# Performance work log

Hardware: AMD Instinct MI355X
Metric: run time of the kernel (lower is better)

The kernel has to match this reference:

```python
import jax, jax.numpy as jnp
import numpy as np
from jax import lax

D_MODEL = 512; D_FF = 2048
D_STATE = 16; D_CONV = 4; EXPAND = 2          # mamba_ssm defaults
D_INNER = EXPAND * D_MODEL                    # 1024
DT_RANK = (D_MODEL + 15) // 16                # 32
B, W, C, D = 2, 1024, 64, 8                   # C*D == D_MODEL


def setup_inputs():
    key = jax.random.key(0)
    ks = jax.random.split(key, 24)
    def p(k, shape, s=0.02):
        return jax.random.normal(k, shape, jnp.float32) * s
    inp = {"x": jax.random.normal(ks[0], (B, W, C, D), jnp.float32)}
    for i, pref in enumerate(["fm", "bm"]):
        o = 1 + i * 7
        inp[pref + "_in_W"] = p(ks[o], (2 * D_INNER, D_MODEL))
        inp[pref + "_conv_W"] = p(ks[o + 1], (D_INNER, D_CONV))
        inp[pref + "_conv_b"] = jnp.zeros((D_INNER,), jnp.float32)
        inp[pref + "_xproj_W"] = p(ks[o + 2], (DT_RANK + 2 * D_STATE, D_INNER))
        inp[pref + "_dt_W"] = p(ks[o + 3], (D_INNER, DT_RANK))
        inp[pref + "_dt_b"] = p(ks[o + 4], (D_INNER,), 0.1)
        inp[pref + "_A_log"] = jnp.log(jnp.broadcast_to(
            jnp.arange(1, D_STATE + 1, dtype=jnp.float32), (D_INNER, D_STATE)))
        inp[pref + "_D"] = jnp.ones((D_INNER,), jnp.float32)
        inp[pref + "_out_W"] = p(ks[o + 5], (D_MODEL, D_INNER))
    inp["ln1_g"] = jnp.ones((D_MODEL,), jnp.float32); inp["ln1_b"] = jnp.zeros((D_MODEL,), jnp.float32)
    inp["ln2_g"] = jnp.ones((D_MODEL,), jnp.float32); inp["ln2_b"] = jnp.zeros((D_MODEL,), jnp.float32)
    inp["ln3_g"] = jnp.ones((D_MODEL,), jnp.float32); inp["ln3_b"] = jnp.zeros((D_MODEL,), jnp.float32)
    inp["ff_W1"] = p(ks[15], (D_FF, D_MODEL)); inp["ff_b1"] = jnp.zeros((D_FF,), jnp.float32)
    inp["ff_W2"] = p(ks[16], (D_MODEL, D_FF)); inp["ff_b2"] = jnp.zeros((D_MODEL,), jnp.float32)
    return inp


def _silu(x):
    return x * jax.nn.sigmoid(x)


def _layernorm(x, g, b, eps=1e-5):
    mu = jnp.mean(x, -1, keepdims=True)
    var = jnp.var(x, -1, keepdims=True)
    return (x - mu) * lax.rsqrt(var + eps) * g + b


def _mamba(u, in_W, conv_W, conv_b, xproj_W, dt_W, dt_b, A_log, Dp, out_W):
    # u: (B, L, d_model). Standard Mamba block (mamba_ssm reference math).
    xz = jnp.einsum('bld,ed->ble', u, in_W)            # (B, L, 2*d_inner)
    xm, z = jnp.split(xz, 2, axis=-1)
    # causal depthwise conv along L
    xc = lax.conv_general_dilated(
        xm.transpose(0, 2, 1), conv_W[:, None, :], (1,),
        [(D_CONV - 1, 0)], feature_group_count=D_INNER)
    xm = _silu((xc + conv_b[None, :, None]).transpose(0, 2, 1))  # (B, L, d_inner)
    dbc = jnp.einsum('bld,ed->ble', xm, xproj_W)       # (B, L, dt_rank + 2*d_state)
    dt = dbc[..., :DT_RANK]
    Bm = dbc[..., DT_RANK:DT_RANK + D_STATE]           # (B, L, d_state)
    Cm = dbc[..., DT_RANK + D_STATE:]                  # (B, L, d_state)
    delta = jax.nn.softplus(jnp.einsum('blr,dr->bld', dt, dt_W) + dt_b)  # (B, L, d_inner)
    A = -jnp.exp(A_log)                                # (d_inner, d_state)
    dA = jnp.exp(delta[..., None] * A)                 # (B, L, d_inner, d_state)
    dBu = delta[..., None] * Bm[:, :, None, :] * xm[..., None]

    def step(h, inputs):
        dA_t, dBu_t = inputs
        h = dA_t * h + dBu_t
        return h, h

    h0 = jnp.zeros((u.shape[0], D_INNER, D_STATE), u.dtype)
    _, hs = lax.scan(step, h0, (dA.transpose(1, 0, 2, 3), dBu.transpose(1, 0, 2, 3)))
    y = jnp.einsum('lbds,lbs->bld', hs, Cm.transpose(1, 0, 2))
    y = y + xm * Dp
    y = y * _silu(z)
    return jnp.einsum('ble,de->bld', y, out_W)         # (B, L, d_model)


def reference(x,
              fm_in_W, fm_conv_W, fm_conv_b, fm_xproj_W, fm_dt_W, fm_dt_b, fm_A_log, fm_D, fm_out_W,
              bm_in_W, bm_conv_W, bm_conv_b, bm_xproj_W, bm_dt_W, bm_dt_b, bm_A_log, bm_D, bm_out_W,
              ln1_g, ln1_b, ln2_g, ln2_b, ln3_g, ln3_b,
              ff_W1, ff_b1, ff_W2, ff_b2):
    b, w, c, d = x.shape
    xf = x.reshape(b, w, c * d)
    fwd = _mamba(xf, fm_in_W, fm_conv_W, fm_conv_b, fm_xproj_W, fm_dt_W, fm_dt_b, fm_A_log, fm_D, fm_out_W)
    bwd = jnp.flip(_mamba(jnp.flip(xf, 1), bm_in_W, bm_conv_W, bm_conv_b, bm_xproj_W,
                          bm_dt_W, bm_dt_b, bm_A_log, bm_D, bm_out_W), 1)
    an1 = _layernorm(xf + fwd, ln1_g, ln1_b)   # AddNorm: LN(x + dropout(y)); dropout off at eval
    an2 = _layernorm(xf + bwd, ln2_g, ln2_b)
    out = an1 + an2
    h = jnp.maximum(jnp.einsum('bld,fd->blf', out, ff_W1) + ff_b1, 0)
    ff = jnp.einsum('blf,df->bld', h, ff_W2) + ff_b2
    out = _layernorm(ff + ff, ln3_g, ln3_b)    # an3(out, out) == LN(out + out)
    return out.reshape(b, w, c, d)
```

## Files before the change

### kernel.cpp

```cpp
#include <hip/hip_runtime.h>
#include <hip/hip_bf16.h>
#include <math.h>

#define MM 2048
#define BATCH 2
#define SEQ 1024
#define DMODEL 512
#define DINNER 1024
#define DSTATE 16
#define DTRANK 32
#define DFF 2048

#define NCHUNK 16
#define CHUNK 64
#define GTOT 65536

typedef short bf16x8 __attribute__((ext_vector_type(8)));
typedef float floatx4 __attribute__((ext_vector_type(4)));
typedef unsigned short ushort8v __attribute__((ext_vector_type(8)));
typedef unsigned short ushort4v __attribute__((ext_vector_type(4)));

__device__ __forceinline__ unsigned short f2bf(float f) {
    union { float f; unsigned u; } v; v.f = f;
    unsigned r = v.u + 0x7FFF + ((v.u >> 16) & 1);
    return (unsigned short)(r >> 16);
}
__device__ __forceinline__ float bf2f(unsigned short u) {
    union { unsigned u; float f; } v; v.u = ((unsigned)u) << 16; return v.f;
}

__device__ __forceinline__ float quadsum4(float x) {
    union { float f; int i; } a, b;
    a.f = x;
    b.i = __builtin_amdgcn_update_dpp(0, a.i, 0xB1, 0xF, 0xF, false); a.f += b.f;
    b.i = __builtin_amdgcn_update_dpp(0, a.i, 0x4E, 0xF, 0xF, false); a.f += b.f;
    return a.f;
}

#define GLOAD_LDS16(gp, lp) __builtin_amdgcn_global_load_lds( \
    (const __attribute__((address_space(1))) unsigned int*)(gp), \
    (__attribute__((address_space(3))) unsigned int*)(lp), 16, 0, 0)


template<int EPI, int OUTBF16>
__global__ __launch_bounds__(256) void gemm_mfma_batch(
    int M, int N, int K,
    const unsigned short* __restrict__ A0, const unsigned short* __restrict__ A1, int lda,
    const unsigned short* __restrict__ B0, const unsigned short* __restrict__ B1, int ldb,
    const float* __restrict__ bias,
    void* __restrict__ C0, void* __restrict__ C1, int ldc)
{
    __shared__ unsigned short As[2][128 * 32];
    __shared__ unsigned short Bs[2][128 * 32];
    const int z = blockIdx.z;
    const unsigned short* A = z ? A1 : A0;
    const unsigned short* B = z ? B1 : B0;
    void* Cout = z ? C1 : C0;
    const int tid  = threadIdx.x;
    const int wave = tid >> 6;
    const int lane = tid & 63;
    const int bm = blockIdx.y * 128;
    const int bn = blockIdx.x * 128;

    const int strow = lane & 15;
    const int stkc  = lane >> 4;
    const int wr = wave >> 1, wc = wave & 1;
    const int frow = lane & 15;
    const int fkc  = lane >> 4;

    floatx4 acc[4][4];
    #pragma unroll
    for (int i = 0; i < 4; ++i)
        #pragma unroll
        for (int j = 0; j < 4; ++j)
            acc[i][j] = (floatx4){0.f, 0.f, 0.f, 0.f};

    for (int k0 = 0; k0 < K; k0 += 64) {
        __syncthreads();
        #pragma unroll
        for (int hh = 0; hh < 2; ++hh) {
            #pragma unroll
            for (int q = 0; q < 2; ++q) {
                int g = wave * 2 + q;
                GLOAD_LDS16(A + (size_t)(bm + g * 16 + strow) * lda + k0 + hh * 32 + stkc * 8,
                            As[hh] + g * 512);
            }
            #pragma unroll
            for (int q = 0; q < 2; ++q) {
                int g = wave * 2 + q;
                GLOAD_LDS16(B + (size_t)(bn + g * 16 + strow) * ldb + k0 + hh * 32 + stkc * 8,
                            Bs[hh] + g * 512);
            }
        }
        __syncthreads();

        #pragma unroll
        for (int hh = 0; hh < 2; ++hh) {
            bf16x8 af[4], bfr[4];
            #pragma unroll
            for (int i = 0; i < 4; ++i)
                af[i] = *(const bf16x8*)(As[hh] + (wr * 4 + i) * 512 + fkc * 128 + frow * 8);
            #pragma unroll
            for (int j = 0; j < 4; ++j)
                bfr[j] = *(const bf16x8*)(Bs[hh] + (wc * 4 + j) * 512 + fkc * 128 + frow * 8);
            #pragma unroll
            for (int i = 0; i < 4; ++i)
                #pragma unroll
                for (int j = 0; j < 4; ++j)
                    acc[i][j] = __builtin_amdgcn_mfma_f32_16x16x32_bf16(
                        af[i], bfr[j], acc[i][j], 0, 0, 0);
        }
    }

    const int orow0 = bm + wr * 64 + (lane >> 4) * 4;
    const int ocol0 = bn + wc * 64 + (lane & 15);
    #pragma unroll
    for (int j = 0; j < 4; ++j) {
        const int col = ocol0 + j * 16;
        const float bv = bias ? bias[col] : 0.f;
        #pragma unroll
        for (int i = 0; i < 4; ++i) {
            #pragma unroll
            for (int r = 0; r < 4; ++r) {
                int row = orow0 + i * 16 + r;
                float t = acc[i][j][r] + bv;
                if (EPI == 1) t = fmaxf(t, 0.f);
                if (OUTBF16)
                    ((unsigned short*)Cout)[(size_t)row * ldc + col] = f2bf(t);
                else
                    ((float*)Cout)[(size_t)row * ldc + col] = t;
            }
        }
    }
}

__global__ __launch_bounds__(256) void gemm_inproj_kernel(
    const unsigned short* __restrict__ A,
    const unsigned short* __restrict__ B0, const unsigned short* __restrict__ B1,
    float* __restrict__ Cx0, float* __restrict__ Cz0,
    float* __restrict__ Cx1, float* __restrict__ Cz1)
{
    __shared__ unsigned short As[2][128 * 32];
    __shared__ unsigned short Bs[2][128 * 32];
    const int z = blockIdx.z;
    const unsigned short* B = z ? B1 : B0;
    const int tid  = threadIdx.x;
    const int wave = tid >> 6;
    const int lane = tid & 63;
    const int bm = blockIdx.y * 128;
    const int bn = blockIdx.x * 128;

    const int strow = lane & 15;
    const int stkc  = lane >> 4;
    const int wr = wave >> 1, wc = wave & 1;
    const int frow = lane & 15;
    const int fkc  = lane >> 4;

    floatx4 acc[4][4];
    #pragma unroll
    for (int i = 0; i < 4; ++i)
        #pragma unroll
        for (int j = 0; j < 4; ++j)
            acc[i][j] = (floatx4){0.f, 0.f, 0.f, 0.f};

    for (int k0 = 0; k0 < DMODEL; k0 += 64) {
        __syncthreads();
        #pragma unroll
        for (int hh = 0; hh < 2; ++hh) {
            #pragma unroll
            for (int q = 0; q < 2; ++q) {
                int g = wave * 2 + q;
                GLOAD_LDS16(A + (size_t)(bm + g * 16 + strow) * DMODEL + k0 + hh * 32 + stkc * 8,
                            As[hh] + g * 512);
            }
            #pragma unroll
            for (int q = 0; q < 2; ++q) {
                int g = wave * 2 + q;
                GLOAD_LDS16(B + (size_t)(bn + g * 16 + strow) * DMODEL + k0 + hh * 32 + stkc * 8,
                            Bs[hh] + g * 512);
            }
        }
        __syncthreads();

        #pragma unroll
        for (int hh = 0; hh < 2; ++hh) {
            bf16x8 af[4], bfr[4];
            #pragma unroll
            for (int i = 0; i < 4; ++i)
                af[i] = *(const bf16x8*)(As[hh] + (wr * 4 + i) * 512 + fkc * 128 + frow * 8);
            #pragma unroll
            for (int j = 0; j < 4; ++j)
                bfr[j] = *(const bf16x8*)(Bs[hh] + (wc * 4 + j) * 512 + fkc * 128 + frow * 8);
            #pragma unroll
            for (int i = 0; i < 4; ++i)
                #pragma unroll
                for (int j = 0; j < 4; ++j)
                    acc[i][j] = __builtin_amdgcn_mfma_f32_16x16x32_bf16(
                        af[i], bfr[j], acc[i][j], 0, 0, 0);
        }
    }

    const int zh = bn >= DINNER;
    float* C = z ? (zh ? Cz1 : Cx1) : (zh ? Cz0 : Cx0);
    const int cb = zh ? DINNER : 0;
    const int orow0 = bm + wr * 64 + (lane >> 4) * 4;
    const int ocol0 = bn + wc * 64 + (lane & 15) - cb;
    #pragma unroll
    for (int j = 0; j < 4; ++j) {
        const int col = ocol0 + j * 16;
        #pragma unroll
        for (int i = 0; i < 4; ++i)
            #pragma unroll
            for (int r = 0; r < 4; ++r)
                C[(size_t)(orow0 + i * 16 + r) * DINNER + col] = acc[i][j][r];
    }
}

template<int NSPLIT>
__global__ __launch_bounds__(256) void gemm_mfma_splitk(
    int M, int N, int K,
    const unsigned short* __restrict__ A0, const unsigned short* __restrict__ A1, int lda,
    const unsigned short* __restrict__ B0, const unsigned short* __restrict__ B1, int ldb,
    float* __restrict__ part, int ldc)
{
    __shared__ unsigned short As[2][128 * 32];
    __shared__ unsigned short Bs[2][128 * 32];
    const int z = blockIdx.z;
    const int dir = z / NSPLIT, sp = z % NSPLIT;
    const unsigned short* A = dir ? A1 : A0;
    const unsigned short* B = dir ? B1 : B0;
    float* Cp = part + (size_t)z * M * ldc;
    const int kbeg = sp * (K / NSPLIT);
    const int kend = kbeg + (K / NSPLIT);
    const int tid  = threadIdx.x;
    const int wave = tid >> 6;
    const int lane = tid & 63;
    const int bm = blockIdx.y * 128;
    const int bn = blockIdx.x * 128;

    const int strow = lane & 15;
    const int stkc  = lane >> 4;
    const int wr = wave >> 1, wc = wave & 1;
    const int frow = lane & 15;
    const int fkc  = lane >> 4;

    floatx4 acc[4][4];
    #pragma unroll
    for (int i = 0; i < 4; ++i)
        #pragma unroll
        for (int j = 0; j < 4; ++j)
            acc[i][j] = (floatx4){0.f, 0.f, 0.f, 0.f};

    for (int k0 = kbeg; k0 < kend; k0 += 64) {
        __syncthreads();
        #pragma unroll
        for (int hh = 0; hh < 2; ++hh) {
            #pragma unroll
            for (int q = 0; q < 2; ++q) {
                int g = wave * 2 + q;
                GLOAD_LDS16(A + (size_t)(bm + g * 16 + strow) * lda + k0 + hh * 32 + stkc * 8,
                            As[hh] + g * 512);
            }
            #pragma unroll
            for (int q = 0; q < 2; ++q) {
                int g = wave * 2 + q;
                GLOAD_LDS16(B + (size_t)(bn + g * 16 + strow) * ldb + k0 + hh * 32 + stkc * 8,
                            Bs[hh] + g * 512);
            }
        }
        __syncthreads();

        #pragma unroll
        for (int hh = 0; hh < 2; ++hh) {
            bf16x8 af[4], bfr[4];
            #pragma unroll
            for (int i = 0; i < 4; ++i)
                af[i] = *(const bf16x8*)(As[hh] + (wr * 4 + i) * 512 + fkc * 128 + frow * 8);
            #pragma unroll
            for (int j = 0; j < 4; ++j)
                bfr[j] = *(const bf16x8*)(Bs[hh] + (wc * 4 + j) * 512 + fkc * 128 + frow * 8);
            #pragma unroll
            for (int i = 0; i < 4; ++i)
                #pragma unroll
                for (int j = 0; j < 4; ++j)
                    acc[i][j] = __builtin_amdgcn_mfma_f32_16x16x32_bf16(
                        af[i], bfr[j], acc[i][j], 0, 0, 0);
        }
    }

    const int orow0 = bm + wr * 64 + (lane >> 4) * 4;
    const int ocol0 = bn + wc * 64 + (lane & 15);
    #pragma unroll
    for (int j = 0; j < 4; ++j) {
        const int col = ocol0 + j * 16;
        #pragma unroll
        for (int i = 0; i < 4; ++i)
            #pragma unroll
            for (int r = 0; r < 4; ++r)
                Cp[(size_t)(orow0 + i * 16 + r) * ldc + col] = acc[i][j][r];
    }
}

__global__ __launch_bounds__(256) void xproj_splitk_kernel(
    const unsigned short* __restrict__ A_f, const unsigned short* __restrict__ A_b,
    const unsigned short* __restrict__ Wf,  const unsigned short* __restrict__ Wb,
    float* __restrict__ part)
{
    __shared__ unsigned short As[2][128 * 32];
    __shared__ unsigned short Bs[2][64 * 32];
    const int tid = threadIdx.x, wave = tid >> 6, lane = tid & 63;
    const int bm = blockIdx.x * 128;
    const int dir = blockIdx.y >> 2, sp = blockIdx.y & 3;
    const unsigned short* A = dir ? A_b : A_f;
    const unsigned short* W = dir ? Wb  : Wf;
    float* Cp = part + (size_t)blockIdx.y * MM * 64;
    const int kbeg = sp * 256, kend = kbeg + 256;

    const int strow = lane & 15;
    const int stkc  = lane >> 4;
    const int frow = lane & 15;
    const int fkc  = lane >> 4;

    floatx4 acc[2][4];
    #pragma unroll
    for (int i = 0; i < 2; ++i)
        #pragma unroll
        for (int j = 0; j < 4; ++j)
            acc[i][j] = (floatx4){0.f, 0.f, 0.f, 0.f};

    for (int k0 = kbeg; k0 < kend; k0 += 64) {
        __syncthreads();
        #pragma unroll
        for (int hh = 0; hh < 2; ++hh) {
            #pragma unroll
            for (int q = 0; q < 2; ++q) {
                int g = wave * 2 + q;
                GLOAD_LDS16(A + (size_t)(bm + g * 16 + strow) * DINNER + k0 + hh * 32 + stkc * 8,
                            As[hh] + g * 512);
            }
            GLOAD_LDS16(W + (size_t)(wave * 16 + strow) * DINNER + k0 + hh * 32 + stkc * 8,
                        Bs[hh] + wave * 512);
        }
        __syncthreads();

        #pragma unroll
        for (int hh = 0; hh < 2; ++hh) {
            bf16x8 af[2], bfr[4];
            #pragma unroll
            for (int i = 0; i < 2; ++i)
                af[i] = *(const bf16x8*)(As[hh] + (wave * 2 + i) * 512 + fkc * 128 + frow * 8);
            #pragma unroll
            for (int j = 0; j < 4; ++j)
                bfr[j] = *(const bf16x8*)(Bs[hh] + j * 512 + fkc * 128 + frow * 8);
            #pragma unroll
            for (int i = 0; i < 2; ++i)
                #pragma unroll
                for (int j = 0; j < 4; ++j)
                    acc[i][j] = __builtin_amdgcn_mfma_f32_16x16x32_bf16(
                        af[i], bfr[j], acc[i][j], 0, 0, 0);
        }
    }

    const int orow0 = bm + wave * 32 + (lane >> 4) * 4;
    #pragma unroll
    for (int j = 0; j < 4; ++j) {
        const int col = (lane & 15) + j * 16;
        #pragma unroll
        for (int i = 0; i < 2; ++i)
            #pragma unroll
            for (int r = 0; r < 4; ++r)
                Cp[(size_t)(orow0 + i * 16 + r) * 64 + col] = acc[i][j][r];
    }
}

__global__ __launch_bounds__(256) void xproj_reduce_kernel(
    const float* __restrict__ part,
    float* __restrict__ dbc_f, float* __restrict__ dbc_b,
    float* __restrict__ bct_f, float* __restrict__ bct_b)
{
    const int dir = blockIdx.y;
    const int i = (blockIdx.x * 256 + threadIdx.x) * 4;
    const float* p = part + (size_t)dir * 4 * (MM * 64);
    float4 a = *(const float4*)(p + i);
    #pragma unroll
    for (int s = 1; s < 4; ++s) {
        float4 t = *(const float4*)(p + (size_t)s * (MM * 64) + i);
        a.x += t.x; a.y += t.y; a.z += t.z; a.w += t.w;
    }
    const int m = i >> 6, c = i & 63;
    if (c < 32) {
        float* dbc = dir ? dbc_b : dbc_f;
        *(float4*)(dbc + (size_t)m * 32 + c) = a;
    } else {
        float* bct = dir ? bct_b : bct_f;
        *(float4*)(bct + (size_t)m * 32 + (c - 32)) = a;
    }
}

__global__ __launch_bounds__(256) void dtproj_batch_kernel(
    int M, int N, int K,
    const float* __restrict__ A0, const float* __restrict__ A1, int lda,
    const float* __restrict__ B0, const float* __restrict__ B1, int ldb,
    const float* __restrict__ bias0, const float* __restrict__ bias1,
    unsigned short* __restrict__ C0, unsigned short* __restrict__ C1, int ldc)
{
    __shared__ float As[16][64];
    __shared__ float Bs[16][64];
    const int z = blockIdx.z;
    const float* A = z ? A1 : A0;
    const float* B = z ? B1 : B0;
    const float* biasR = z ? bias1 : bias0;
    unsigned short* C = z ? C1 : C0;
    const int tid = threadIdx.x;
    const int tx = tid & 15, ty = tid >> 4;
    const int bm = blockIdx.y * 64, bn = blockIdx.x * 64;
    const int lm = tid & 63;
    const int lk = (tid >> 6) * 4;
    const float* Arow = A + (size_t)(bm + lm) * lda + lk;
    const float* Brow = B + (size_t)(bn + lm) * ldb + lk;
    float acc[4][4] = {};
    for (int k0 = 0; k0 < K; k0 += 16) {
        float4 av = *(const float4*)(Arow + k0);
        float4 bv = *(const float4*)(Brow + k0);
        __syncthreads();
        As[lk+0][lm] = av.x; As[lk+1][lm] = av.y; As[lk+2][lm] = av.z; As[lk+3][lm] = av.w;
        Bs[lk+0][lm] = bv.x; Bs[lk+1][lm] = bv.y; Bs[lk+2][lm] = bv.z; Bs[lk+3][lm] = bv.w;
        __syncthreads();
        #pragma unroll
        for (int k = 0; k < 16; ++k) {
            float4 a = *(const float4*)(&As[k][ty*4]);
            float4 b = *(const float4*)(&Bs[k][tx*4]);
            float ar[4] = {a.x,a.y,a.z,a.w};
            float br[4] = {b.x,b.y,b.z,b.w};
            #pragma unroll
            for (int i = 0; i < 4; ++i)
                #pragma unroll
                for (int j = 0; j < 4; ++j)
                    acc[i][j] = fmaf(ar[i], br[j], acc[i][j]);
        }
    }
    const int row0 = bm + ty*4, col0 = bn + tx*4;
    #pragma unroll
    for (int i = 0; i < 4; ++i) {
        float br = biasR[row0 + i];
        ushort4v o;
        #pragma unroll
        for (int j = 0; j < 4; ++j) {
            float t = acc[i][j] + br;
            o[j] = f2bf(fmaxf(t, 0.f) + log1pf(__expf(-fabsf(t))));
        }
        *(ushort4v*)(C + (size_t)(row0 + i) * ldc + col0) = o;
    }
}

__global__ __launch_bounds__(256) void cast_pre_kernel(
    const float* __restrict__ x, const float* __restrict__ w0,
    const float* __restrict__ w1, const float* __restrict__ xp0,
    const float* __restrict__ xp1, unsigned short* __restrict__ dst)
{
    int i = (blockIdx.x * 256 + threadIdx.x) * 8;
    const float* src; int off;
    if      (i < 1048576) { src = x;   off = 0; }
    else if (i < 2097152) { src = w0;  off = 1048576; }
    else if (i < 3145728) { src = w1;  off = 2097152; }
    else if (i < 3211264) { src = xp0; off = 3145728; }
    else                  { src = xp1; off = 3211264; }
    float4 a = *(const float4*)(src + i - off);
    float4 b = *(const float4*)(src + i - off + 4);
    ushort8v o;
    o[0] = f2bf(a.x); o[1] = f2bf(a.y); o[2] = f2bf(a.z); o[3] = f2bf(a.w);
    o[4] = f2bf(b.x); o[5] = f2bf(b.y); o[6] = f2bf(b.z); o[7] = f2bf(b.w);
    *(ushort8v*)(dst + i) = o;
}

__global__ __launch_bounds__(256) void cast_post_kernel(
    const float* __restrict__ w0, const float* __restrict__ w1,
    const float* __restrict__ w2, const float* __restrict__ w3,
    unsigned short* __restrict__ dst)
{
    int i = (blockIdx.x * 256 + threadIdx.x) * 8;
    const float* src; int off;
    if      (i < 524288)  { src = w0; off = 0; }
    else if (i < 1048576) { src = w1; off = 524288; }
    else if (i < 2097152) { src = w2; off = 1048576; }
    else                  { src = w3; off = 2097152; }
    float4 a = *(const float4*)(src + i - off);
    float4 b = *(const float4*)(src + i - off + 4);
    ushort8v o;
    o[0] = f2bf(a.x); o[1] = f2bf(a.y); o[2] = f2bf(a.z); o[3] = f2bf(a.w);
    o[4] = f2bf(b.x); o[5] = f2bf(b.y); o[6] = f2bf(b.z); o[7] = f2bf(b.w);
    *(ushort8v*)(dst + i) = o;
}

__global__ __launch_bounds__(256) void conv_silu_tr_kernel(
    const float* __restrict__ x_f, const float* __restrict__ x_b,
    const float* __restrict__ Wf,  const float* __restrict__ Wb,
    const float* __restrict__ cbf, const float* __restrict__ cbb,
    unsigned short* __restrict__ of,  unsigned short* __restrict__ ob,
    unsigned short* __restrict__ otf, unsigned short* __restrict__ otb)
{
    __shared__ unsigned short t[32][34];
    const int dir = blockIdx.z;
    const float* xo = dir ? x_b : x_f;
    const float* convW = dir ? Wb : Wf;
    const float* convb = dir ? cbb : cbf;
    unsigned short* xm  = dir ? ob : of;
    unsigned short* xmT = dir ? otb : otf;
    const int m0 = blockIdx.x * 32, d0 = blockIdx.y * 32;
    const int tx = threadIdx.x & 31, ty = threadIdx.x >> 5;
    const int d = d0 + tx;
    float4 wv = *(const float4*)(convW + d * 4);
    float w[4] = {wv.x, wv.y, wv.z, wv.w};
    const float cb = convb[d];
    #pragma unroll
    for (int rr = 0; rr < 32; rr += 8) {
        int m = m0 + ty + rr;
        int b = m >> 10, l = m & (SEQ - 1);
        float acc = cb;
        #pragma unroll
        for (int j = 0; j < 4; ++j) {
            int p = dir ? (l + 3 - j) : (l - 3 + j);
            if (p >= 0 && p < SEQ)
                acc = fmaf(xo[(size_t)(b * SEQ + p) * DINNER + d], w[j], acc);
        }
        float sig = 1.f / (1.f + __expf(-acc));
        unsigned short v = f2bf(acc * sig);
        xm[(size_t)m * DINNER + d] = v;
        t[ty + rr][tx] = v;
    }
    __syncthreads();
    #pragma unroll
    for (int rr = 0; rr < 32; rr += 8)
        xmT[(size_t)(d0 + ty + rr) * MM + m0 + tx] = t[tx][ty + rr];
}

template<int DIR>
__device__ __forceinline__ void pass1_body(
    const unsigned short* __restrict__ deltaT, const unsigned short* __restrict__ xmT,
    const float* __restrict__ bct, const float* __restrict__ Alog,
    const float* __restrict__ Dv,
    unsigned short* __restrict__ y0T, float* __restrict__ cumT,
    float* __restrict__ Pout, float* __restrict__ Hout)
{
    const int tid = threadIdx.x;
    const int sq = tid & 3;
    const int dloc = tid >> 2;
    const int d = blockIdx.x * 64 + dloc;
    const int b = blockIdx.y / NCHUNK;
    const int c = blockIdx.y % NCHUNK;

    float4 Av = *(const float4*)(Alog + d * DSTATE + sq * 4);
    const float A0 = -__expf(Av.x), A1 = -__expf(Av.y);
    const float A2 = -__expf(Av.z), A3 = -__expf(Av.w);
    const float Dp = Dv[d];
    const unsigned short* dRow = deltaT + (size_t)d * MM + b * SEQ;
    const unsigned short* xRow = xmT + (size_t)d * MM + b * SEQ;
    const float* bcRow = bct + (size_t)(b * SEQ) * 32 + sq * 4;
    unsigned short* yRow = y0T + (size_t)d * MM + b * SEQ;
    float* uRow = cumT + (size_t)d * MM + b * SEQ;

    float h0 = 0.f, h1 = 0.f, h2 = 0.f, h3 = 0.f, sdl = 0.f;
    const int segBase = DIR ? (SEQ - CHUNK - c * CHUNK) : (c * CHUNK);
    for (int ii = 0; ii < CHUNK; ii += 8) {
        const int off = DIR ? (segBase + (CHUNK - 8) - ii) : (segBase + ii);
        ushort8v dl8 = *(const ushort8v*)(dRow + off);
        ushort8v x8  = *(const ushort8v*)(xRow + off);
        float yv[8], cu[8];
        #pragma unroll
        for (int u = 0; u < 8; ++u) {
            const int t = DIR ? (7 - u) : u;
            float4 Bv = *(const float4*)(bcRow + (size_t)(off + t) * 32);
            float4 Cv = *(const float4*)(bcRow + (size_t)(off + t) * 32 + 16);
            float dlv = bf2f(dl8[t]);
            float xv  = bf2f(x8[t]);
            sdl += dlv;
            float dx = dlv * xv;
            h0 = fmaf(__expf(dlv * A0), h0, dx * Bv.x);
            h1 = fmaf(__expf(dlv * A1), h1, dx * Bv.y);
            h2 = fmaf(__expf(dlv * A2), h2, dx * Bv.z);
            h3 = fmaf(__expf(dlv * A3), h3, dx * Bv.w);
            float part = h0 * Cv.x + h1 * Cv.y + h2 * Cv.z + h3 * Cv.w;
            part = quadsum4(part);
            yv[t] = fmaf(xv, Dp, part);
            cu[t] = sdl;
        }
        if (sq == 0) {
            ushort8v y8;
            #pragma unroll
            for (int u = 0; u < 8; ++u) y8[u] = f2bf(yv[u]);
            *(ushort8v*)(yRow + off) = y8;
            *(float4*)(uRow + off)     = (float4){cu[0], cu[1], cu[2], cu[3]};
            *(float4*)(uRow + off + 4) = (float4){cu[4], cu[5], cu[6], cu[7]};
        }
    }
    const size_t g4 = ((size_t)(DIR * BATCH + b) * DINNER + d) * DSTATE + sq * 4;
    *(float4*)(Pout + (size_t)c * GTOT + g4) =
        (float4){__expf(sdl * A0), __expf(sdl * A1), __expf(sdl * A2), __expf(sdl * A3)};
    *(float4*)(Hout + (size_t)c * GTOT + g4) = (float4){h0, h1, h2, h3};
}

__global__ __launch_bounds__(256) void scan_pass1_kernel(
    const unsigned short* __restrict__ dT_f, const unsigned short* __restrict__ dT_b,
    const unsigned short* __restrict__ xT_f, const unsigned short* __restrict__ xT_b,
    const float* __restrict__ bct_f, const float* __restrict__ bct_b,
    const float* __restrict__ Alog_f, const float* __restrict__ Alog_b,
    const float* __restrict__ D_f, const float* __restrict__ D_b,
    unsigned short* __restrict__ y0T_f, unsigned short* __restrict__ y0T_b,
    float* __restrict__ cumT_f, float* __restrict__ cumT_b,
    float* __restrict__ Pout, float* __restrict__ Hout)
{
    if (blockIdx.z == 0)
        pass1_body<0>(dT_f, xT_f, bct_f, Alog_f, D_f, y0T_f, cumT_f, Pout, Hout);
    else
        pass1_body<1>(dT_b, xT_b, bct_b, Alog_b, D_b, y0T_b, cumT_b, Pout, Hout);
}

__global__ __launch_bounds__(256) void scan_carry_kernel(
    const float* __restrict__ P, const float* __restrict__ H,
    float* __restrict__ carry)
{
    const int g = blockIdx.x * 256 + threadIdx.x;
    float p[NCHUNK], hh[NCHUNK];
    #pragma unroll
    for (int c = 0; c < NCHUNK; ++c) {
        p[c]  = P[(size_t)c * GTOT + g];
        hh[c] = H[(size_t)c * GTOT + g];
    }
    float h = 0.f;
    #pragma unroll
    for (int c = 0; c < NCHUNK; ++c) {
        carry[(size_t)c * GTOT + g] = h;
        h = fmaf(p[c], h, hh[c]);
    }
}

__global__ __launch_bounds__(256) void scan_correct_kernel(
    const unsigned short* __restrict__ y0T_f, const unsigned short* __restrict__ y0T_b,
    const float* __restrict__ cumT_f, const float* __restrict__ cumT_b,
    const float* __restrict__ bct_f, const float* __restrict__ bct_b,
    const float* __restrict__ Alog_f, const float* __restrict__ Alog_b,
    const float* __restrict__ carry,
    const float* __restrict__ z_f, const float* __restrict__ z_b,
    unsigned short* __restrict__ ybf_f, unsigned short* __restrict__ ybf_b)
{
    __shared__ float Cs[16][33];
    __shared__ float Asm[32][16];
    __shared__ float Cy[32][16];
    __shared__ float t[32][33];

    const int dir = blockIdx.z;
    const unsigned short* y0T = dir ? y0T_b : y0T_f;
    const float* cumT = dir ? cumT_b : cumT_f;
    const float* bct  = dir ? bct_b  : bct_f;
    const float* Alog = dir ? Alog_b : Alog_f;
    const float* zon  = dir ? z_b    : z_f;
    unsigned short* ybf = dir ? ybf_b : ybf_f;

    const int m0 = blockIdx.x * 32, d0 = blockIdx.y * 32;
    const int b = m0 >> 10;
    const int l0 = m0 & (SEQ - 1);
    const int c = dir ? ((SEQ - 1 - l0) >> 6) : (l0 >> 6);

    for (int idx = threadIdx.x; idx < 512; idx += 256) {
        int s1 = idx & 15, ml = idx >> 4;
        Cs[s1][ml] = bct[(size_t)(m0 + ml) * 32 + 16 + s1];
        int dl2 = idx >> 4, s2 = idx & 15;
        Asm[dl2][s2] = -__expf(Alog[(d0 + dl2) * DSTATE + s2]);
        Cy[dl2][s2] = carry[(size_t)c * GTOT
            + ((size_t)(dir * BATCH + b) * DINNER + d0 + dl2) * DSTATE + s2];
    }
    __syncthreads();

    const int tx = threadIdx.x & 31, ty = threadIdx.x >> 5;
    #pragma unroll
    for (int rr = 0; rr < 32; rr += 8) {
        const int dloc = ty + rr;
        const size_t base = (size_t)(d0 + dloc) * MM + m0 + tx;
        float u  = cumT[base];
        float y0 = bf2f(y0T[base]);
        float corr = 0.f;
        #pragma unroll
        for (int s = 0; s < DSTATE; ++s)
            corr = fmaf(Cs[s][tx] * Cy[dloc][s], __expf(Asm[dloc][s] * u), corr);
        t[dloc][tx] = y0 + corr;
    }
    __syncthreads();
    #pragma unroll
    for (int rr = 0; rr < 32; rr += 8) {
        int m = m0 + ty + rr, d = d0 + tx;
        float z = zon[(size_t)m * DINNER + d];
        float sig = 1.f / (1.f + __expf(-z));
        ybf[(size_t)m * DINNER + d] = f2bf(t[tx][ty + rr] * (z * sig));
    }
}

__global__ __launch_bounds__(256) void ln_combine_fused_kernel(
    const float* __restrict__ xf, const float* __restrict__ part,
    const float* __restrict__ g1, const float* __restrict__ b1,
    const float* __restrict__ g2, const float* __restrict__ b2,
    unsigned short* __restrict__ out)
{
    const int m = blockIdx.x;
    const int tid = threadIdx.x;
    const float* xr = xf + (size_t)m * DMODEL;
    const float* p0 = part + (size_t)m * DMODEL;
    const float* p1 = p0 + (size_t)MM * DMODEL;
    const float* p2 = p1 + (size_t)MM * DMODEL;
    const float* p3 = p2 + (size_t)MM * DMODEL;
    float v1a = xr[tid]       + p0[tid]       + p1[tid];
    float v1b = xr[tid + 256] + p0[tid + 256] + p1[tid + 256];
    float v2a = xr[tid]       + p2[tid]       + p3[tid];
    float v2b = xr[tid + 256] + p2[tid + 256] + p3[tid + 256];
    float s1 = v1a + v1b, q1 = v1a*v1a + v1b*v1b;
    float s2 = v2a + v2b, q2 = v2a*v2a + v2b*v2b;
    #pragma unroll
    for (int off = 32; off; off >>= 1) {
        s1 += __shfl_xor(s1, off); q1 += __shfl_xor(q1, off);
        s2 += __shfl_xor(s2, off); q2 += __shfl_xor(q2, off);
    }
    __shared__ float sm[4][4];
    const int w = tid >> 6;
    if ((tid & 63) == 0) { sm[w][0] = s1; sm[w][1] = q1; sm[w][2] = s2; sm[w][3] = q2; }
    __syncthreads();
    s1 = sm[0][0] + sm[1][0] + sm[2][0] + sm[3][0];
    q1 = sm[0][1] + sm[1][1] + sm[2][1] + sm[3][1];
    s2 = sm[0][2] + sm[1][2] + sm[2][2] + sm[3][2];
    q2 = sm[0][3] + sm[1][3] + sm[2][3] + sm[3][3];
    const float inv = 1.f / DMODEL;
    float mu1 = s1 * inv, mu2 = s2 * inv;
    float rs1 = rsqrtf(q1 * inv - mu1 * mu1 + 1e-5f);
    float rs2 = rsqrtf(q2 * inv - mu2 * mu2 + 1e-5f);
    unsigned short* orow = out + (size_t)m * DMODEL;
    orow[tid]       = f2bf((v1a - mu1) * rs1 * g1[tid]       + b1[tid]
                         + (v2a - mu2) * rs2 * g2[tid]       + b2[tid]);
    orow[tid + 256] = f2bf((v1b - mu1) * rs1 * g1[tid + 256] + b1[tid + 256]
                         + (v2b - mu2) * rs2 * g2[tid + 256] + b2[tid + 256]);
}

__global__ __launch_bounds__(256) void ln_final_fused_kernel(
    const float* __restrict__ part, const float* __restrict__ bias,
    const float* __restrict__ g, const float* __restrict__ b,
    float* __restrict__ out)
{
    const int m = blockIdx.x;
    const int tid = threadIdx.x;
    const size_t stride = (size_t)MM * DMODEL;
    const float* p = part + (size_t)m * DMODEL;
    float fa = bias[tid]       + p[tid]       + p[stride + tid]
             + p[2*stride + tid]       + p[3*stride + tid];
    float fb = bias[tid + 256] + p[tid + 256] + p[stride + tid + 256]
             + p[2*stride + tid + 256] + p[3*stride + tid + 256];
    float va = 2.f * fa, vb = 2.f * fb;
    float s = va + vb, q = va*va + vb*vb;
    #pragma unroll
    for (int off = 32; off; off >>= 1) {
        s += __shfl_xor(s, off); q += __shfl_xor(q, off);
    }
    __shared__ float sm[4][2];
    const int w = tid >> 6;
    if ((tid & 63) == 0) { sm[w][0] = s; sm[w][1] = q; }
    __syncthreads();
    s = sm[0][0] + sm[1][0] + sm[2][0] + sm[3][0];
    q = sm[0][1] + sm[1][1] + sm[2][1] + sm[3][1];
    const float inv = 1.f / DMODEL;
    float mu = s * inv;
    float rs = rsqrtf(q * inv - mu * mu + 1e-5f);
    float* orow = out + (size_t)m * DMODEL;
    orow[tid]       = (va - mu) * rs * g[tid]       + b[tid];
    orow[tid + 256] = (vb - mu) * rs * g[tid + 256] + b[tid + 256];
}

extern "C" void kernel_launch(void* const* d_in, const int* in_sizes, int n_in,
                              void* d_out, int out_size, void* d_ws, size_t ws_size,
                              hipStream_t stream)
{
    const float* x         = (const float*)d_in[0];
    const float* fm_in_W   = (const float*)d_in[1];
    const float* fm_conv_W = (const float*)d_in[2];
    const float* fm_conv_b = (const float*)d_in[3];
    const float* fm_xproj_W= (const float*)d_in[4];
    const float* fm_dt_W   = (const float*)d_in[5];
    const float* fm_dt_b   = (const float*)d_in[6];
    const float* fm_A_log  = (const float*)d_in[7];
    const float* fm_D      = (const float*)d_in[8];
    const float* fm_out_W  = (const float*)d_in[9];
    const float* bm_in_W   = (const float*)d_in[10];
    const float* bm_conv_W = (const float*)d_in[11];
    const float* bm_conv_b = (const float*)d_in[12];
    const float* bm_xproj_W= (const float*)d_in[13];
    const float* bm_dt_W   = (const float*)d_in[14];
    const float* bm_dt_b   = (const float*)d_in[15];
    const float* bm_A_log  = (const float*)d_in[16];
    const float* bm_D      = (const float*)d_in[17];
    const float* bm_out_W  = (const float*)d_in[18];
    const float* ln1_g     = (const float*)d_in[19];
    const float* ln1_b     = (const float*)d_in[20];
    const float* ln2_g     = (const float*)d_in[21];
    const float* ln2_b     = (const float*)d_in[22];
    const float* ln3_g     = (const float*)d_in[23];
    const float* ln3_b     = (const float*)d_in[24];
    const float* ff_W1     = (const float*)d_in[25];
    const float* ff_b1     = (const float*)d_in[26];
    const float* ff_W2     = (const float*)d_in[27];
    const float* ff_b2     = (const float*)d_in[28];
    float* out = (float*)d_out;

    float* ws = (float*)d_ws;
    size_t o = 0;
    float* xonly_f = ws + o; o += (size_t)MM * DINNER;
    float* xonly_b = ws + o; o += (size_t)MM * DINNER;
    float* zonly_f = ws + o; o += (size_t)MM * DINNER;
    float* zonly_b = ws + o; o += (size_t)MM * DINNER;
    unsigned short* xm_bf_f = (unsigned short*)(ws + o); o += (size_t)MM * DINNER / 2;
    unsigned short* xm_bf_b = (unsigned short*)(ws + o); o += (size_t)MM * DINNER / 2;
    unsigned short* xmT_f   = (unsigned short*)(ws + o); o += (size_t)MM * DINNER / 2;
    unsigned short* xmT_b   = (unsigned short*)(ws + o); o += (size_t)MM * DINNER / 2;
    unsigned short* deltaT_f= (unsigned short*)(ws + o); o += (size_t)MM * DINNER / 2;
    unsigned short* deltaT_b= (unsigned short*)(ws + o); o += (size_t)MM * DINNER / 2;
    float* dbc_f    = ws + o; o += (size_t)MM * 32;
    float* dbc_b    = ws + o; o += (size_t)MM * 32;
    float* bct_f    = ws + o; o += (size_t)MM * 32;
    float* bct_b    = ws + o; o += (size_t)MM * 32;
    unsigned short* y0T_f = (unsigned short*)(ws + o); o += (size_t)MM * DINNER / 2;
    unsigned short* y0T_b = (unsigned short*)(ws + o); o += (size_t)MM * DINNER / 2;
    float* scanP    = ws + o; o += (size_t)NCHUNK * (GTOT / 16) * 16;
    float* scanH    = ws + o; o += (size_t)NCHUNK * (GTOT / 16) * 16;
    float* scanCy   = ws + o; o += (size_t)NCHUNK * (GTOT / 16) * 16;
    float* gpart    = ws + o; o += (size_t)4 * MM * DMODEL;

    float* cumT_f = xonly_f;
    float* cumT_b = xonly_b;
    unsigned short* x_bf       = (unsigned short*)scanP;
    unsigned short* fm_inW_bf  = x_bf + 1048576;
    unsigned short* bm_inW_bf  = fm_inW_bf + 1048576;
    unsigned short* fm_xpW_bf  = bm_inW_bf + 1048576;
    unsigned short* bm_xpW_bf  = fm_xpW_bf + 65536;
    unsigned short* ybf_f = (unsigned short*)scanP;
    unsigned short* ybf_b = (unsigned short*)scanH;
    unsigned short* fm_outW_bf = (unsigned short*)zonly_f;
    unsigned short* bm_outW_bf = fm_outW_bf + 524288;
    unsigned short* W1_bf      = bm_outW_bf + 524288;
    unsigned short* W2_bf      = W1_bf + 1048576;
    unsigned short* outsum_bf  = (unsigned short*)xonly_b;
    unsigned short* h_bf = (unsigned short*)deltaT_f;

    cast_pre_kernel<<<3276800 / 2048, 256, 0, stream>>>(
        x, fm_in_W, bm_in_W, fm_xproj_W, bm_xproj_W, x_bf);

    gemm_inproj_kernel<<<dim3(2048/128, MM/128, 2), 256, 0, stream>>>(
        x_bf, fm_inW_bf, bm_inW_bf, xonly_f, zonly_f, xonly_b, zonly_b);

    conv_silu_tr_kernel<<<dim3(MM/32, DINNER/32, 2), 256, 0, stream>>>(
        xonly_f, xonly_b, fm_conv_W, bm_conv_W, fm_conv_b, bm_conv_b,
        xm_bf_f, xm_bf_b, xmT_f, xmT_b);

    xproj_splitk_kernel<<<dim3(MM/128, 8), 256, 0, stream>>>(
        xm_bf_f, xm_bf_b, fm_xpW_bf, bm_xpW_bf, gpart);
    xproj_reduce_kernel<<<dim3((MM*64)/1024, 2), 256, 0, stream>>>(
        gpart, dbc_f, dbc_b, bct_f, bct_b);

    dtproj_batch_kernel<<<dim3(MM/64, DINNER/64, 2), 256, 0, stream>>>(
        DINNER, MM, DTRANK, fm_dt_W, bm_dt_W, DTRANK, dbc_f, dbc_b, 32,
        fm_dt_b, bm_dt_b, deltaT_f, deltaT_b, MM);

    scan_pass1_kernel<<<dim3(DINNER/64, BATCH*NCHUNK, 2), 256, 0, stream>>>(
        deltaT_f, deltaT_b, xmT_f, xmT_b, bct_f, bct_b,
        fm_A_log, bm_A_log, fm_D, bm_D,
        y0T_f, y0T_b, cumT_f, cumT_b, scanP, scanH);
    scan_carry_kernel<<<GTOT/256, 256, 0, stream>>>(scanP, scanH, scanCy);
    scan_correct_kernel<<<dim3(MM/32, DINNER/32, 2), 256, 0, stream>>>(
        y0T_f, y0T_b, cumT_f, cumT_b, bct_f, bct_b, fm_A_log, bm_A_log,
        scanCy, zonly_f, zonly_b, ybf_f, ybf_b);

    cast_post_kernel<<<3145728 / 2048, 256, 0, stream>>>(
        fm_out_W, bm_out_W, ff_W1, ff_W2, fm_outW_bf);

    gemm_mfma_splitk<2><<<dim3(DMODEL/128, MM/128, 4), 256, 0, stream>>>(
        MM, DMODEL, DINNER, ybf_f, ybf_b, DINNER, fm_outW_bf, bm_outW_bf, DINNER,
        gpart, DMODEL);

    ln_combine_fused_kernel<<<MM, 256, 0, stream>>>(
        x, gpart, ln1_g, ln1_b, ln2_g, ln2_b, outsum_bf);

    gemm_mfma_batch<1,1><<<dim3(DFF/128, MM/128, 1), 256, 0, stream>>>(
        MM, DFF, DMODEL, outsum_bf, outsum_bf, DMODEL, W1_bf, W1_bf, DMODEL,
        ff_b1, h_bf, h_bf, DFF);

    gemm_mfma_splitk<4><<<dim3(DMODEL/128, MM/128, 4), 256, 0, stream>>>(
        MM, DMODEL, DFF, h_bf, h_bf, DFF, W2_bf, W2_bf, DFF, gpart, DMODEL);

    ln_final_fused_kernel<<<MM, 256, 0, stream>>>(
        gpart, ff_b2, ln3_g, ln3_b, out);
}
```

Baseline: 305.5 us.

## Store in-proj outputs as bf16 and raise split-K across projection GEMMs

The in-projection GEMM now writes x and z as bf16 rather than fp32, and the conv and scan-correct kernels read them as bf16. This halves the traffic for those intermediates. The out-projection and FF2 GEMMs raise split-K from 2→4 and 4→8, and FF1 moves from a fused-epilogue GEMM to split-K 2 followed by a separate bias/ReLU reduce kernel, putting more blocks on the GPU. The cost is extra partial-sum traffic in fp32 and one more launch, and the workspace layout is reshuffled so cumT now aliases the enlarged gpart buffer.

```diff
diff --git a/kernel.cpp b/kernel.cpp
--- a/kernel.cpp
+++ b/kernel.cpp
@@ -137,8 +137,8 @@
 __global__ __launch_bounds__(256) void gemm_inproj_kernel(
     const unsigned short* __restrict__ A,
     const unsigned short* __restrict__ B0, const unsigned short* __restrict__ B1,
-    float* __restrict__ Cx0, float* __restrict__ Cz0,
-    float* __restrict__ Cx1, float* __restrict__ Cz1)
+    unsigned short* __restrict__ Cx0, unsigned short* __restrict__ Cz0,
+    unsigned short* __restrict__ Cx1, unsigned short* __restrict__ Cz1)
 {
     __shared__ unsigned short As[2][128 * 32];
     __shared__ unsigned short Bs[2][128 * 32];
@@ -201,7 +201,7 @@
     }
 
     const int zh = bn >= DINNER;
-    float* C = z ? (zh ? Cz1 : Cx1) : (zh ? Cz0 : Cx0);
+    unsigned short* C = z ? (zh ? Cz1 : Cx1) : (zh ? Cz0 : Cx0);
     const int cb = zh ? DINNER : 0;
     const int orow0 = bm + wr * 64 + (lane >> 4) * 4;
     const int ocol0 = bn + wc * 64 + (lane & 15) - cb;
@@ -212,7 +212,7 @@
         for (int i = 0; i < 4; ++i)
             #pragma unroll
             for (int r = 0; r < 4; ++r)
-                C[(size_t)(orow0 + i * 16 + r) * DINNER + col] = acc[i][j][r];
+                C[(size_t)(orow0 + i * 16 + r) * DINNER + col] = f2bf(acc[i][j][r]);
     }
 }
 
@@ -493,7 +493,7 @@
 }
 
 __global__ __launch_bounds__(256) void conv_silu_tr_kernel(
-    const float* __restrict__ x_f, const float* __restrict__ x_b,
+    const unsigned short* __restrict__ x_f, const unsigned short* __restrict__ x_b,
     const float* __restrict__ Wf,  const float* __restrict__ Wb,
     const float* __restrict__ cbf, const float* __restrict__ cbb,
     unsigned short* __restrict__ of,  unsigned short* __restrict__ ob,
@@ -501,7 +501,7 @@
 {
     __shared__ unsigned short t[32][34];
     const int dir = blockIdx.z;
-    const float* xo = dir ? x_b : x_f;
+    const unsigned short* xo = dir ? x_b : x_f;
     const float* convW = dir ? Wb : Wf;
     const float* convb = dir ? cbb : cbf;
     unsigned short* xm  = dir ? ob : of;
@@ -521,7 +521,7 @@
         for (int j = 0; j < 4; ++j) {
             int p = dir ? (l + 3 - j) : (l - 3 + j);
             if (p >= 0 && p < SEQ)
-                acc = fmaf(xo[(size_t)(b * SEQ + p) * DINNER + d], w[j], acc);
+                acc = fmaf(bf2f(xo[(size_t)(b * SEQ + p) * DINNER + d]), w[j], acc);
         }
         float sig = 1.f / (1.f + __expf(-acc));
         unsigned short v = f2bf(acc * sig);
@@ -640,7 +640,7 @@
     const float* __restrict__ bct_f, const float* __restrict__ bct_b,
     const float* __restrict__ Alog_f, const float* __restrict__ Alog_b,
     const float* __restrict__ carry,
-    const float* __restrict__ z_f, const float* __restrict__ z_b,
+    const unsigned short* __restrict__ z_f, const unsigned short* __restrict__ z_b,
     unsigned short* __restrict__ ybf_f, unsigned short* __restrict__ ybf_b)
 {
     __shared__ float Cs[16][33];
@@ -653,7 +653,7 @@
     const float* cumT = dir ? cumT_b : cumT_f;
     const float* bct  = dir ? bct_b  : bct_f;
     const float* Alog = dir ? Alog_b : Alog_f;
-    const float* zon  = dir ? z_b    : z_f;
+    const unsigned short* zon = dir ? z_b : z_f;
     unsigned short* ybf = dir ? ybf_b : ybf_f;
 
     const int m0 = blockIdx.x * 32, d0 = blockIdx.y * 32;
@@ -688,10 +688,26 @@
     #pragma unroll
     for (int rr = 0; rr < 32; rr += 8) {
         int m = m0 + ty + rr, d = d0 + tx;
-        float z = zon[(size_t)m * DINNER + d];
+        float z = bf2f(zon[(size_t)m * DINNER + d]);
         float sig = 1.f / (1.f + __expf(-z));
         ybf[(size_t)m * DINNER + d] = f2bf(t[tx][ty + rr] * (z * sig));
     }
+}
+
+__global__ __launch_bounds__(256) void reduce_ff1_kernel(
+    const float* __restrict__ part, const float* __restrict__ bias,
+    unsigned short* __restrict__ outh)
+{
+    const int i = (blockIdx.x * 256 + threadIdx.x) * 4;
+    float4 a = *(const float4*)(part + i);
+    float4 b = *(const float4*)(part + (size_t)MM * DFF + i);
+    const int c = i & (DFF - 1);
+    ushort4v o;
+    o[0] = f2bf(fmaxf(a.x + b.x + bias[c],     0.f));
+    o[1] = f2bf(fmaxf(a.y + b.y + bias[c + 1], 0.f));
+    o[2] = f2bf(fmaxf(a.z + b.z + bias[c + 2], 0.f));
+    o[3] = f2bf(fmaxf(a.w + b.w + bias[c + 3], 0.f));
+    *(ushort4v*)(outh + i) = o;
 }
 
 __global__ __launch_bounds__(256) void ln_combine_fused_kernel(
@@ -702,15 +718,16 @@
 {
     const int m = blockIdx.x;
     const int tid = threadIdx.x;
+    const size_t stride = (size_t)MM * DMODEL;
     const float* xr = xf + (size_t)m * DMODEL;
-    const float* p0 = part + (size_t)m * DMODEL;
-    const float* p1 = p0 + (size_t)MM * DMODEL;
-    const float* p2 = p1 + (size_t)MM * DMODEL;
-    const float* p3 = p2 + (size_t)MM * DMODEL;
-    float v1a = xr[tid]       + p0[tid]       + p1[tid];
-    float v1b = xr[tid + 256] + p0[tid + 256] + p1[tid + 256];
-    float v2a = xr[tid]       + p2[tid]       + p3[tid];
-    float v2b = xr[tid + 256] + p2[tid + 256] + p3[tid + 256];
+    const float* p = part + (size_t)m * DMODEL;
+    float v1a = xr[tid], v1b = xr[tid + 256];
+    float v2a = xr[tid], v2b = xr[tid + 256];
+    #pragma unroll
+    for (int k = 0; k < 4; ++k) {
+        v1a += p[k * stride + tid];       v1b += p[k * stride + tid + 256];
+        v2a += p[(4 + k) * stride + tid]; v2b += p[(4 + k) * stride + tid + 256];
+    }
     float s1 = v1a + v1b, q1 = v1a*v1a + v1b*v1b;
     float s2 = v2a + v2b, q2 = v2a*v2a + v2b*v2b;
     #pragma unroll
@@ -746,10 +763,12 @@
     const int tid = threadIdx.x;
     const size_t stride = (size_t)MM * DMODEL;
     const float* p = part + (size_t)m * DMODEL;
-    float fa = bias[tid]       + p[tid]       + p[stride + tid]
-             + p[2*stride + tid]       + p[3*stride + tid];
-    float fb = bias[tid + 256] + p[tid + 256] + p[stride + tid + 256]
-             + p[2*stride + tid + 256] + p[3*stride + tid + 256];
+    float fa = bias[tid], fb = bias[tid + 256];
+    #pragma unroll
+    for (int k = 0; k < 8; ++k) {
+        fa += p[k * stride + tid];
+        fb += p[k * stride + tid + 256];
+    }
     float va = 2.f * fa, vb = 2.f * fb;
     float s = va + vb, q = va*va + vb*vb;
     #pragma unroll
@@ -807,10 +826,10 @@
 
     float* ws = (float*)d_ws;
     size_t o = 0;
-    float* xonly_f = ws + o; o += (size_t)MM * DINNER;
-    float* xonly_b = ws + o; o += (size_t)MM * DINNER;
-    float* zonly_f = ws + o; o += (size_t)MM * DINNER;
-    float* zonly_b = ws + o; o += (size_t)MM * DINNER;
+    unsigned short* xbf_f = (unsigned short*)(ws + o); o += (size_t)MM * DINNER / 2;
+    unsigned short* xbf_b = (unsigned short*)(ws + o); o += (size_t)MM * DINNER / 2;
+    unsigned short* zbf_f = (unsigned short*)(ws + o); o += (size_t)MM * DINNER / 2;
+    unsigned short* zbf_b = (unsigned short*)(ws + o); o += (size_t)MM * DINNER / 2;
     unsigned short* xm_bf_f = (unsigned short*)(ws + o); o += (size_t)MM * DINNER / 2;
     unsigned short* xm_bf_b = (unsigned short*)(ws + o); o += (size_t)MM * DINNER / 2;
     unsigned short* xmT_f   = (unsigned short*)(ws + o); o += (size_t)MM * DINNER / 2;
@@ -826,32 +845,32 @@
     float* scanP    = ws + o; o += (size_t)NCHUNK * (GTOT / 16) * 16;
     float* scanH    = ws + o; o += (size_t)NCHUNK * (GTOT / 16) * 16;
     float* scanCy   = ws + o; o += (size_t)NCHUNK * (GTOT / 16) * 16;
-    float* gpart    = ws + o; o += (size_t)4 * MM * DMODEL;
-
-    float* cumT_f = xonly_f;
-    float* cumT_b = xonly_b;
-    unsigned short* x_bf       = (unsigned short*)scanP;
-    unsigned short* fm_inW_bf  = x_bf + 1048576;
+    float* gpart    = ws + o; o += (size_t)8 * MM * DMODEL;
+
+    float* cumT_f = gpart;
+    float* cumT_b = gpart + (size_t)MM * DINNER;
+    unsigned short* xin_bf     = (unsigned short*)scanP;
+    unsigned short* fm_inW_bf  = xin_bf + 1048576;
     unsigned short* bm_inW_bf  = fm_inW_bf + 1048576;
     unsigned short* fm_xpW_bf  = bm_inW_bf + 1048576;
     unsigned short* bm_xpW_bf  = fm_xpW_bf + 65536;
     unsigned short* ybf_f = (unsigned short*)scanP;
     unsigned short* ybf_b = (unsigned short*)scanH;
-    unsigned short* fm_outW_bf = (unsigned short*)zonly_f;
+    unsigned short* fm_outW_bf = (unsigned short*)zbf_f;
     unsigned short* bm_outW_bf = fm_outW_bf + 524288;
     unsigned short* W1_bf      = bm_outW_bf + 524288;
     unsigned short* W2_bf      = W1_bf + 1048576;
-    unsigned short* outsum_bf  = (unsigned short*)xonly_b;
+    unsigned short* outsum_bf  = (unsigned short*)xbf_f;
     unsigned short* h_bf = (unsigned short*)deltaT_f;
 
     cast_pre_kernel<<<3276800 / 2048, 256, 0, stream>>>(
-        x, fm_in_W, bm_in_W, fm_xproj_W, bm_xproj_W, x_bf);
+        x, fm_in_W, bm_in_W, fm_xproj_W, bm_xproj_W, xin_bf);
 
     gemm_inproj_kernel<<<dim3(2048/128, MM/128, 2), 256, 0, stream>>>(
-        x_bf, fm_inW_bf, bm_inW_bf, xonly_f, zonly_f, xonly_b, zonly_b);
+        xin_bf, fm_inW_bf, bm_inW_bf, xbf_f, zbf_f, xbf_b, zbf_b);
 
     conv_silu_tr_kernel<<<dim3(MM/32, DINNER/32, 2), 256, 0, stream>>>(
-        xonly_f, xonly_b, fm_conv_W, bm_conv_W, fm_conv_b, bm_conv_b,
+        xbf_f, xbf_b, fm_conv_W, bm_conv_W, fm_conv_b, bm_conv_b,
         xm_bf_f, xm_bf_b, xmT_f, xmT_b);
 
     xproj_splitk_kernel<<<dim3(MM/128, 8), 256, 0, stream>>>(
@@ -870,23 +889,24 @@
     scan_carry_kernel<<<GTOT/256, 256, 0, stream>>>(scanP, scanH, scanCy);
     scan_correct_kernel<<<dim3(MM/32, DINNER/32, 2), 256, 0, stream>>>(
         y0T_f, y0T_b, cumT_f, cumT_b, bct_f, bct_b, fm_A_log, bm_A_log,
-        scanCy, zonly_f, zonly_b, ybf_f, ybf_b);
+        scanCy, zbf_f, zbf_b, ybf_f, ybf_b);
 
     cast_post_kernel<<<3145728 / 2048, 256, 0, stream>>>(
         fm_out_W, bm_out_W, ff_W1, ff_W2, fm_outW_bf);
 
-    gemm_mfma_splitk<2><<<dim3(DMODEL/128, MM/128, 4), 256, 0, stream>>>(
+    gemm_mfma_splitk<4><<<dim3(DMODEL/128, MM/128, 8), 256, 0, stream>>>(
         MM, DMODEL, DINNER, ybf_f, ybf_b, DINNER, fm_outW_bf, bm_outW_bf, DINNER,
         gpart, DMODEL);
 
     ln_combine_fused_kernel<<<MM, 256, 0, stream>>>(
         x, gpart, ln1_g, ln1_b, ln2_g, ln2_b, outsum_bf);
 
-    gemm_mfma_batch<1,1><<<dim3(DFF/128, MM/128, 1), 256, 0, stream>>>(
+    gemm_mfma_splitk<2><<<dim3(DFF/128, MM/128, 2), 256, 0, stream>>>(
         MM, DFF, DMODEL, outsum_bf, outsum_bf, DMODEL, W1_bf, W1_bf, DMODEL,
-        ff_b1, h_bf, h_bf, DFF);
-
-    gemm_mfma_splitk<4><<<dim3(DMODEL/128, MM/128, 4), 256, 0, stream>>>(
+        gpart, DFF);
+    reduce_ff1_kernel<<<(MM*DFF)/1024, 256, 0, stream>>>(gpart, ff_b1, h_bf);
+
+    gemm_mfma_splitk<8><<<dim3(DMODEL/128, MM/128, 8), 256, 0, stream>>>(
         MM, DMODEL, DFF, h_bf, h_bf, DFF, W2_bf, W2_bf, DFF, gpart, DMODEL);
 
     ln_final_fused_kernel<<<MM, 256, 0, stream>>>(
```

After: 308.1 us. Within noise of the previous version (+0.9%).
